# Kernel optimization log

Hardware: AMD Instinct MI355X
Metric: run time of the kernel (lower is better)

## Reference

```python
import jax, jax.numpy as jnp
import numpy as np

D_MODEL = 512; N_LAYERS = 12; D_STATE = 64; D_CONV = 4; EXPAND = 2
HEADDIM = 64; KLEN = 10
D_INNER = EXPAND * D_MODEL              # 1024
NHEADS = D_INNER // HEADDIM             # 16
CONV_DIM = D_INNER + 2 * D_STATE        # 1152
D_IN_PROJ = 2 * D_INNER + 2 * D_STATE + NHEADS  # 2192
CHUNK = 128; EPS = 1e-5
B_SZ = 2; SEQ = 2048


def rmsnorm(x, w):
    return x * jax.lax.rsqrt(jnp.mean(x * x, axis=-1, keepdims=True) + EPS) * w


def nerf_pe(x):
    # NeRF positional encoding of raw 3D coords, zero-padded to D_MODEL
    nf = D_MODEL // (2 * x.shape[-1])  # 85 freqs per coord -> 510 dims
    freqs = 2.0 ** jnp.arange(nf, dtype=x.dtype)
    ang = x[..., None] * freqs                       # [B,L,3,nf]
    pe = jnp.concatenate([jnp.sin(ang), jnp.cos(ang)], axis=-1)
    pe = pe.reshape(*x.shape[:-1], -1)               # [B,L,510]
    return jnp.pad(pe, ((0, 0), (0, 0), (0, D_MODEL - pe.shape[-1])))


def ssd(xh, dt, A, Bm, Cm):
    # Chunked Mamba2 SSD selective scan.
    # xh [B,L,H,P], dt [B,L,H] (post-softplus), A [H] (negative), Bm/Cm [B,L,N]
    Bb, L, H, P = xh.shape; N = Bm.shape[-1]; C = L // CHUNK
    xh = xh.reshape(Bb, C, CHUNK, H, P)
    dt = dt.reshape(Bb, C, CHUNK, H)
    Bm = Bm.reshape(Bb, C, CHUNK, N)
    Cm = Cm.reshape(Bb, C, CHUNK, N)
    a = dt * A                                   # [B,C,Q,H], <= 0
    a_cum = jnp.cumsum(a, axis=2)
    # intra-chunk decay L[i,j] = exp(a_cum_i - a_cum_j), i >= j
    diff = a_cum[:, :, :, None, :] - a_cum[:, :, None, :, :]  # [B,C,i,j,H]
    tri = jnp.tril(jnp.ones((CHUNK, CHUNK), bool))
    Lmat = jnp.where(tri[None, None, :, :, None], jnp.exp(diff), 0.0)
    scores = jnp.einsum('bcin,bcjn->bcij', Cm, Bm)
    M = scores[..., None] * Lmat * dt[:, :, None, :, :]       # [B,C,i,j,H]
    y_diag = jnp.einsum('bcijh,bcjhp->bcihp', M, xh)
    # per-chunk end states
    a_sum = a_cum[:, :, -1, :]                                # [B,C,H]
    dstate = jnp.exp(a_sum[:, :, None, :] - a_cum) * dt       # [B,C,Q,H]
    S = jnp.einsum('bcjh,bcjn,bcjhp->bchpn', dstate, Bm, xh)  # [B,C,H,P,N]
    dec = jnp.exp(a_sum)

    def step(h, inp):
        Sc, dc = inp
        return h * dc[:, :, None, None] + Sc, h  # emit state BEFORE this chunk

    h0 = jnp.zeros((Bb, H, P, N), xh.dtype)
    _, hs = jax.lax.scan(step, h0, (S.transpose(1, 0, 2, 3, 4), dec.transpose(1, 0, 2)))
    y_off = jnp.einsum('bcih,bcin,cbhpn->bcihp', jnp.exp(a_cum), Cm, hs)
    return (y_diag + y_off).reshape(Bb, L, H, P)


def mamba_block(x, in_w, conv_w, conv_b, dt_b, A_log, Dp, gw, out_w):
    Bb, L, _ = x.shape
    zxbcdt = x @ in_w                             # [B,L,2192]
    z = zxbcdt[..., :D_INNER]
    xBC = zxbcdt[..., D_INNER:D_INNER + CONV_DIM]
    dt = zxbcdt[..., D_INNER + CONV_DIM:]
    # causal depthwise conv1d, kernel D_CONV
    xp = jnp.pad(xBC, ((0, 0), (D_CONV - 1, 0), (0, 0)))
    xc = sum(xp[:, k:k + L, :] * conv_w[:, k] for k in range(D_CONV)) + conv_b
    xc = jax.nn.silu(xc)
    xh = xc[..., :D_INNER].reshape(Bb, L, NHEADS, HEADDIM)
    Bm = xc[..., D_INNER:D_INNER + D_STATE]
    Cm = xc[..., D_INNER + D_STATE:]
    dt = jax.nn.softplus(dt + dt_b)
    A = -jnp.exp(A_log)
    y = ssd(xh, dt, A, Bm, Cm) + Dp[None, None, :, None] * xh
    y = y.reshape(Bb, L, D_INNER)
    y = rmsnorm(y * jax.nn.silu(z), gw)           # gated RMSNorm
    return y @ out_w


def setup_inputs() -> dict:
    key = jax.random.key(0)
    ks = jax.random.split(key, 8)
    s = 0.02
    x = jax.random.normal(ks[0], (B_SZ, SEQ, 3), jnp.float32)
    W_embed = jax.random.normal(ks[1], (3, D_MODEL), jnp.float32) * s
    rms_w = jnp.ones((N_LAYERS, D_MODEL), jnp.float32)
    in_proj_w = jax.random.normal(ks[2], (N_LAYERS, D_MODEL, D_IN_PROJ), jnp.float32) * s
    conv_w = jax.random.normal(ks[3], (N_LAYERS, CONV_DIM, D_CONV), jnp.float32) * s
    conv_b = jnp.zeros((N_LAYERS, CONV_DIM), jnp.float32)
    dt_bias = jax.random.normal(ks[4], (N_LAYERS, NHEADS), jnp.float32) * 0.1
    A_log = jnp.log(jnp.broadcast_to(jnp.arange(1, NHEADS + 1, dtype=jnp.float32), (N_LAYERS, NHEADS)))
    D_param = jnp.ones((N_LAYERS, NHEADS), jnp.float32)
    gnorm_w = jnp.ones((N_LAYERS, D_INNER), jnp.float32)
    out_proj_w = jax.random.normal(ks[5], (N_LAYERS, D_INNER, D_MODEL), jnp.float32) * s
    final_norm_w = jnp.ones((D_MODEL,), jnp.float32)
    head_w = jax.random.normal(ks[6], (D_MODEL, KLEN * 3), jnp.float32) * s
    head_b = jnp.zeros((KLEN * 3,), jnp.float32)
    return dict(x=x, W_embed=W_embed, rms_w=rms_w, in_proj_w=in_proj_w,
                conv_w=conv_w, conv_b=conv_b, dt_bias=dt_bias, A_log=A_log,
                D_param=D_param, gnorm_w=gnorm_w, out_proj_w=out_proj_w,
                final_norm_w=final_norm_w, head_w=head_w, head_b=head_b)


def reference(x, W_embed, rms_w, in_proj_w, conv_w, conv_b, dt_bias, A_log,
              D_param, gnorm_w, out_proj_w, final_norm_w, head_w, head_b):
    x = jnp.where(x == -100.0, 0.0, x)            # change_maskval
    h = x @ W_embed + nerf_pe(x)                  # EmbedderAdd

    def layer(h, p):
        rw, iw, cw, cb, db, al, dp, gw, ow = p
        z = mamba_block(rmsnorm(h, rw), iw, cw, cb, db, al, dp, gw, ow)
        return h + z, None                        # dropout is identity in eval

    h, _ = jax.lax.scan(layer, h, (rms_w, in_proj_w, conv_w, conv_b, dt_bias,
                                   A_log, D_param, gnorm_w, out_proj_w))
    h = rmsnorm(h, final_norm_w)
    return h @ head_w + head_b                    # [B,L,30]
```

## Files before the change

### kernel.cpp

```cpp
#include <hip/hip_runtime.h>
#include <math.h>

#define DM 512
#define DSTATE 64
#define HD 64
#define DI 1024
#define NH 16
#define CONVD 1152
#define DIP 2192
#define CHK 128
#define NCH 16
#define BSZ 2
#define SEQL 2048
#define BL (BSZ*SEQL)
#define NLAYER 12
#define EPSF 1e-5f
#define NPAD_IN 2304

typedef __attribute__((ext_vector_type(4))) float f32x4;
typedef __attribute__((ext_vector_type(8))) short s16x8;

__device__ __forceinline__ float bf2f(ushort u) {
    union { unsigned int i; float f; } v; v.i = ((unsigned int)u) << 16; return v.f;
}
__device__ __forceinline__ ushort f2bf(float f) {
    union { float f; unsigned int u; } v; v.f = f;
    unsigned int u = v.u;
    unsigned int r = (u + 0x7fffu + ((u >> 16) & 1u)) >> 16;
    return (ushort)r;
}

#define GLOAD_LDS16(gptr, lptr) __builtin_amdgcn_global_load_lds( \
    (const __attribute__((address_space(1))) void*)(gptr), \
    (__attribute__((address_space(3))) void*)(lptr), 16, 0, 0)

#define MFMA_BF16(a, b, c) __builtin_amdgcn_mfma_f32_16x16x32_bf16(a, b, c, 0, 0, 0)

__global__ void embed_kernel(const float* __restrict__ x, const float* __restrict__ W,
                             float* __restrict__ h) {
    int tok = blockIdx.x;
    float xe[3];
#pragma unroll
    for (int e = 0; e < 3; e++) {
        float v = x[tok * 3 + e];
        xe[e] = (v == -100.0f) ? 0.0f : v;
    }
    for (int d = threadIdx.x; d < DM; d += blockDim.x) {
        float pe = 0.0f;
        if (d < 510) {
            int e = d / 170, r = d % 170;
            int is_sin = (r < 85);
            int k = is_sin ? r : r - 85;
            float ang = xe[e] * ldexpf(1.0f, k);
            double dv = is_sin ? sin((double)ang) : cos((double)ang);
            pe = (float)dv;
        }
        float acc = pe;
#pragma unroll
        for (int e = 0; e < 3; e++) acc += xe[e] * W[e * DM + d];
        h[(size_t)tok * DM + d] = acc;
    }
}

__global__ __launch_bounds__(256) void rmsnorm512_bf_kernel(const float* __restrict__ in,
                                                            const float* __restrict__ w,
                                                            ushort* __restrict__ out) {
    int tok = blockIdx.x;
    const float* row = in + (size_t)tok * DM;
    float v0 = row[threadIdx.x];
    float v1 = row[threadIdx.x + 256];
    float ss = v0 * v0 + v1 * v1;
    for (int o = 32; o; o >>= 1) ss += __shfl_down(ss, o);
    __shared__ float sbuf[4];
    if ((threadIdx.x & 63) == 0) sbuf[threadIdx.x >> 6] = ss;
    __syncthreads();
    if (threadIdx.x == 0) {
        float s = sbuf[0] + sbuf[1] + sbuf[2] + sbuf[3];
        sbuf[0] = rsqrtf(s / (float)DM + EPSF);
    }
    __syncthreads();
    float rs = sbuf[0];
    ushort* orow = out + (size_t)tok * DM;
    orow[threadIdx.x] = f2bf(v0 * rs * w[threadIdx.x]);
    orow[threadIdx.x + 256] = f2bf(v1 * rs * w[threadIdx.x + 256]);
}

__global__ __launch_bounds__(256) void gatenorm_kernel(const float* __restrict__ y,
                                                       const ushort* __restrict__ zx,
                                                       const float* __restrict__ gw,
                                                       ushort* __restrict__ yb) {
    int tok = blockIdx.x;
    const ushort* zrow = zx + (size_t)tok * DIP;
    const float* yrow = y + (size_t)tok * DI;
    float v[4];
    float ss = 0.0f;
#pragma unroll
    for (int k = 0; k < 4; k++) {
        int d = threadIdx.x + k * 256;
        float z = bf2f(zrow[d]);
        float s = z / (1.0f + __expf(-z));
        float val = yrow[d] * s;
        v[k] = val;
        ss += val * val;
    }
    for (int o = 32; o; o >>= 1) ss += __shfl_down(ss, o);
    __shared__ float sbuf[4];
    if ((threadIdx.x & 63) == 0) sbuf[threadIdx.x >> 6] = ss;
    __syncthreads();
    if (threadIdx.x == 0) {
        float s = sbuf[0] + sbuf[1] + sbuf[2] + sbuf[3];
        sbuf[0] = rsqrtf(s / (float)DI + EPSF);
    }
    __syncthreads();
    float rs = sbuf[0];
    ushort* ob = yb + (size_t)tok * DI;
#pragma unroll
    for (int k = 0; k < 4; k++) {
        int d = threadIdx.x + k * 256;
        ob[d] = f2bf(v[k] * rs * gw[d]);
    }
}

__global__ __launch_bounds__(256) void convT_kernel(const float* __restrict__ w,
                                                    ushort* __restrict__ wT,
                                                    int K, int N, int Npad) {
    __shared__ ushort tile[64][65];
    int l = blockIdx.z;
    int n0 = blockIdx.x * 64, k0 = blockIdx.y * 64;
    const float* src = w + (size_t)l * K * N;
    ushort* dst = wT + (size_t)l * Npad * K;
    int tid = threadIdx.x;
#pragma unroll
    for (int t = 0; t < 16; t++) {
        int idx = tid + t * 256;
        int r = idx >> 6, c = idx & 63;
        float v = (n0 + c < N) ? src[(size_t)(k0 + r) * N + n0 + c] : 0.0f;
        tile[c][r] = f2bf(v);
    }
    __syncthreads();
#pragma unroll
    for (int t = 0; t < 16; t++) {
        int idx = tid + t * 256;
        int r = idx >> 6, c = idx & 63;
        dst[(size_t)(n0 + r) * K + k0 + c] = tile[r][c];
    }
}

template <int MODE, int MT>
__global__ __launch_bounds__(256) void gemm_bf16_kernel(
    const ushort* __restrict__ A, const ushort* __restrict__ BT,
    ushort* __restrict__ Cb, float* __restrict__ Cf, float* __restrict__ aux,
    int N, int Nstride, int K)
{
    __shared__ ushort As[2][MT * 32 * 64];
    __shared__ ushort Bs[2][128 * 64];
    int nwg = gridDim.x * gridDim.y;
    int w0 = blockIdx.y * gridDim.x + blockIdx.x;
    int wg = (w0 & 7) * (nwg >> 3) + (w0 >> 3);
    int by = wg / gridDim.x, bx = wg - by * gridDim.x;
    int bm = by * (MT * 32), bn = bx * 128;
    int tid = threadIdx.x;
    int lane = tid & 63, wid = tid >> 6;
    int wr = wid >> 1, wc = wid & 1;
    int r15 = lane & 15, q = lane >> 4;
    f32x4 acc[MT][4] = {};
    const int nkt = K >> 6;

#define STAGE_GEMM(b, kt) do {                                              \
        int k0s = (kt) << 6;                                                \
        _Pragma("unroll")                                                   \
        for (int t = 0; t < MT; t++) {                                      \
            int cbase = wid * (MT * 64) + t * 64;                           \
            int chunk = cbase + lane;                                       \
            int row = chunk >> 3, s = chunk & 7;                            \
            int kc = s ^ (row & 7);                                         \
            GLOAD_LDS16(A + (size_t)(bm + row) * K + k0s + kc * 8,          \
                        &As[b][cbase * 8]);                                 \
        }                                                                   \
        _Pragma("unroll")                                                   \
        for (int t = 0; t < 4; t++) {                                       \
            int cbase = wid * 256 + t * 64;                                 \
            int chunk = cbase + lane;                                       \
            int row = chunk >> 3, s = chunk & 7;                            \
            int kc = s ^ (row & 7);                                         \
            GLOAD_LDS16(BT + (size_t)(bn + row) * K + k0s + kc * 8,         \
                        &Bs[b][cbase * 8]);                                 \
        }                                                                   \
    } while (0)

    STAGE_GEMM(0, 0);
    __syncthreads();
    for (int kt = 0; kt < nkt; kt++) {
        int cur = kt & 1;
        if (kt + 1 < nkt) STAGE_GEMM(cur ^ 1, kt + 1);
        const ushort* Ac = As[cur];
        const ushort* Bc = Bs[cur];
#pragma unroll
        for (int kh = 0; kh < 2; kh++) {
            s16x8 av[MT], bv[4];
#pragma unroll
            for (int m = 0; m < MT; m++) {
                int row = wr * (MT * 16) + m * 16 + r15;
                int s = (kh * 4 + q) ^ (row & 7);
                av[m] = *(const s16x8*)(Ac + row * 64 + s * 8);
            }
#pragma unroll
            for (int n = 0; n < 4; n++) {
                int row = wc * 64 + n * 16 + r15;
                int s = (kh * 4 + q) ^ (row & 7);
                bv[n] = *(const s16x8*)(Bc + row * 64 + s * 8);
            }
#pragma unroll
            for (int m = 0; m < MT; m++)
#pragma unroll
                for (int n = 0; n < 4; n++)
                    acc[m][n] = MFMA_BF16(av[m], bv[n], acc[m][n]);
        }
        __syncthreads();
    }
#undef STAGE_GEMM

#pragma unroll
    for (int m = 0; m < MT; m++) {
        int row0 = bm + wr * (MT * 16) + m * 16 + q * 4;
#pragma unroll
        for (int n = 0; n < 4; n++) {
            int col = bn + wc * 64 + n * 16 + r15;
#pragma unroll
            for (int r = 0; r < 4; r++) {
                float v = acc[m][n][r];
                int rr = row0 + r;
                if (MODE == 0) {
                    if (col < N) {
                        Cb[(size_t)rr * Nstride + col] = f2bf(v);
                        if (col >= DI + CONVD) aux[(size_t)rr * 16 + (col - DI - CONVD)] = v;
                    }
                } else if (MODE == 1) {
                    Cf[(size_t)rr * Nstride + col] += v;
                } else {
                    if (col < N) Cf[(size_t)rr * Nstride + col] = v + aux[col];
                }
            }
        }
    }
}

__global__ __launch_bounds__(256) void conv_kernel(const ushort* __restrict__ zx,
                                                   const float* __restrict__ cw,
                                                   const float* __restrict__ cb,
                                                   ushort* __restrict__ xc) {
    int gid = blockIdx.x * 256 + threadIdx.x;
    int cu = gid % (CONVD / 8);
    int rb = gid / (CONVD / 8);
    int c8 = cu * 8;
    int l0 = rb * 4;
    int lmod = l0 & (SEQL - 1);

    float wk[4][8];
    const float4* wp = (const float4*)(cw + c8 * 4);
#pragma unroll
    for (int e = 0; e < 8; e++) {
        float4 v = wp[e];
        wk[0][e] = v.x; wk[1][e] = v.y; wk[2][e] = v.z; wk[3][e] = v.w;
    }
    float4 b0 = *(const float4*)(cb + c8);
    float4 b1 = *(const float4*)(cb + c8 + 4);
    float bias[8] = {b0.x, b0.y, b0.z, b0.w, b1.x, b1.y, b1.z, b1.w};

    const ushort* base = zx + (size_t)l0 * DIP + DI + c8;
    s16x8 zero = {};
    s16x8 rows[7];
    rows[0] = (lmod >= 3) ? *(const s16x8*)(base - 3 * DIP) : zero;
    rows[1] = (lmod >= 2) ? *(const s16x8*)(base - 2 * DIP) : zero;
    rows[2] = (lmod >= 1) ? *(const s16x8*)(base - 1 * DIP) : zero;
#pragma unroll
    for (int r = 0; r < 4; r++) rows[3 + r] = *(const s16x8*)(base + (size_t)r * DIP);

    ushort* ob = xc + (size_t)l0 * CONVD + c8;
#pragma unroll
    for (int r = 0; r < 4; r++) {
        s16x8 o;
#pragma unroll
        for (int e = 0; e < 8; e++) {
            float a = bias[e];
#pragma unroll
            for (int k = 0; k < 4; k++)
                a += bf2f((ushort)rows[r + k][e]) * wk[k][e];
            float s = a / (1.0f + __expf(-a));
            o[e] = (short)f2bf(s);
        }
        *(s16x8*)(ob + (size_t)r * CONVD) = o;
    }
}

__global__ __launch_bounds__(512, 4) void ssd1_kernel(
    const ushort* __restrict__ xc, const float* __restrict__ dtraw,
    const float* __restrict__ dt_bias, const float* __restrict__ A_log,
    const float* __restrict__ Dp, float* __restrict__ acg,
    float* __restrict__ decbuf, float* __restrict__ y, float* __restrict__ S)
{
    __shared__ ushort Mb[128 * 128];
    __shared__ ushort xhT[64 * 136];
    __shared__ ushort BmT[64 * 136];
    __shared__ float sAc[128], sDt[128], sDs[128];
    __shared__ float s_wsum, s_stot;

    int hh = blockIdx.x, bc = blockIdx.y;
    int tid = threadIdx.x, lane = tid & 63, w = tid >> 6;
    int l15 = lane & 15, lq = lane >> 4;
    int bch = bc * NH + hh;
    const size_t xbase = (size_t)(bc * CHK) * CONVD;
    ushort* Cs = Mb;
    ushort* Bs = Mb + 8192;

#pragma unroll
    for (int t = 0; t < 2; t++) {
        int cbase = t * 512 + w * 64;
        int chunk = cbase + lane;
        int row = chunk >> 3, s = chunk & 7;
        int kc = s ^ (row & 7);
        GLOAD_LDS16(xc + xbase + (size_t)row * CONVD + DI + DSTATE + kc * 8, Cs + (size_t)cbase * 8);
        GLOAD_LDS16(xc + xbase + (size_t)row * CONVD + DI + kc * 8, Bs + (size_t)cbase * 8);
    }
    {
        int j = tid & 127, pc = tid >> 7;
#pragma unroll
        for (int it = 0; it < 2; it++) {
            int pc8 = pc * 2 + it;
            s16x8 vx = *(const s16x8*)(xc + xbase + (size_t)j * CONVD + hh * HD + pc8 * 8);
            s16x8 vb = *(const s16x8*)(xc + xbase + (size_t)j * CONVD + DI + pc8 * 8);
#pragma unroll
            for (int e = 0; e < 8; e++) {
                int R = pc8 * 8 + e;
                int off = R * 136 + (((j >> 3) ^ (R & 7)) << 3) + (j & 7);
                xhT[off] = (ushort)vx[e];
                BmT[off] = (ushort)vb[e];
            }
        }
    }
    float v_scan = 0.0f, dt_v = 0.0f;
    if (tid < 128) {
        float raw = dtraw[(size_t)(bc * CHK + tid) * 16 + hh] + dt_bias[hh];
        dt_v = raw > 0.0f ? raw + log1pf(__expf(-raw)) : log1pf(__expf(raw));
        v_scan = dt_v * (-__expf(A_log[hh]));
#pragma unroll
        for (int o = 1; o < 64; o <<= 1) {
            float u = __shfl_up(v_scan, o);
            if (lane >= o) v_scan += u;
        }
        if (tid == 63) s_wsum = v_scan;
    }
    __syncthreads();

    float ac_v = 0.0f;
    if (tid < 128) {
        ac_v = (tid >= 64) ? v_scan + s_wsum : v_scan;
        if (tid == 127) s_stot = ac_v;
    }
    f32x4 acc_s[8] = {};
    {
        int row = w * 16 + l15;
#pragma unroll
        for (int kh = 0; kh < 2; kh++) {
            int sl = (kh * 4 + lq) ^ (row & 7);
            s16x8 av = *(const s16x8*)(Cs + row * 64 + sl * 8);
#pragma unroll
            for (int nj = 0; nj < 8; nj++) {
                int jr = nj * 16 + l15;
                int sl2 = (kh * 4 + lq) ^ (jr & 7);
                s16x8 bv = *(const s16x8*)(Bs + jr * 64 + sl2 * 8);
                acc_s[nj] = MFMA_BF16(av, bv, acc_s[nj]);
            }
        }
    }
    __syncthreads();

    if (tid < 128) {
        float asum = s_stot;
        sAc[tid] = ac_v;
        sDt[tid] = dt_v;
        sDs[tid] = __expf(asum - ac_v) * dt_v;
        acg[(size_t)bch * CHK + tid] = ac_v;
        if (tid == 0) decbuf[bch] = __expf(asum);
    }
    __syncthreads();

#pragma unroll
    for (int nj = 0; nj < 8; nj++) {
        int j = nj * 16 + l15;
        if (nj < w) {
            float acj = sAc[j], dtj = sDt[j];
#pragma unroll
            for (int r = 0; r < 4; r++) {
                int i = w * 16 + lq * 4 + r;
                float v = acc_s[nj][r] * __expf(sAc[i] - acj) * dtj;
                Mb[i * 128 + ((((i & 7) ^ (j >> 3)) << 3) | (j & 7))] = f2bf(v);
            }
        } else if (nj == w) {
            float acj = sAc[j], dtj = sDt[j];
#pragma unroll
            for (int r = 0; r < 4; r++) {
                int i = w * 16 + lq * 4 + r;
                float v = (j <= i) ? acc_s[nj][r] * __expf(sAc[i] - acj) * dtj : 0.0f;
                Mb[i * 128 + ((((i & 7) ^ (j >> 3)) << 3) | (j & 7))] = f2bf(v);
            }
        } else if (nj == w + 1) {
#pragma unroll
            for (int r = 0; r < 4; r++) {
                int i = w * 16 + lq * 4 + r;
                Mb[i * 128 + ((((i & 7) ^ (j >> 3)) << 3) | (j & 7))] = 0;
            }
        }
    }
    __syncthreads();

    int ph = w >> 2, iq = w & 3;
    f32x4 acc_y[2][2] = {};
    f32x4 acc_st[2] = {};
    int nn = iq * 16 + l15;
#pragma unroll
    for (int ks = 0; ks < 4; ks++) {
        int cj = ks * 4 + lq;
        int j0 = ks * 32 + lq * 8;
        s16x8 axh[2], axs[2];
#pragma unroll
        for (int m = 0; m < 2; m++) {
            int p = ph * 32 + m * 16 + l15;
            axh[m] = *(const s16x8*)(xhT + p * 136 + ((cj ^ (p & 7)) << 3));
            s16x8 r;
#pragma unroll
            for (int e = 0; e < 8; e++)
                r[e] = (short)f2bf(bf2f((ushort)axh[m][e]) * sDs[j0 + e]);
            axs[m] = r;
        }
        s16x8 bb = *(const s16x8*)(BmT + nn * 136 + ((cj ^ (nn & 7)) << 3));
#pragma unroll
        for (int m = 0; m < 2; m++)
            acc_st[m] = MFMA_BF16(axs[m], bb, acc_st[m]);
        if (ks <= iq) {
            s16x8 bm_[2];
#pragma unroll
            for (int n = 0; n < 2; n++) {
                int i = iq * 32 + n * 16 + l15;
                bm_[n] = *(const s16x8*)(Mb + i * 128 + ((cj ^ (i & 7)) << 3));
            }
#pragma unroll
            for (int m = 0; m < 2; m++)
#pragma unroll
                for (int n = 0; n < 2; n++)
                    acc_y[m][n] = MFMA_BF16(axh[m], bm_[n], acc_y[m][n]);
        }
    }

    float Dh = Dp[hh];
#pragma unroll
    for (int m = 0; m < 2; m++) {
        int p0 = ph * 32 + m * 16 + lq * 4;
#pragma unroll
        for (int n = 0; n < 2; n++) {
            int i = iq * 32 + n * 16 + l15;
            f32x4 v = acc_y[m][n];
#pragma unroll
            for (int r = 0; r < 4; r++) {
                int p = p0 + r;
                v[r] += Dh * bf2f(xhT[p * 136 + ((((p & 7) ^ (i >> 3)) << 3) | (i & 7))]);
            }
            *(f32x4*)&y[(size_t)(bc * CHK + i) * DI + hh * HD + p0] = v;
        }
#pragma unroll
        for (int r = 0; r < 4; r++)
            S[(size_t)bch * 4096 + (size_t)(p0 + r) * 64 + nn] = acc_st[m][r];
    }
}

__global__ void scan_kernel(const float* __restrict__ S, const float* __restrict__ decbuf,
                            float* __restrict__ hs) {
    int g = blockIdx.x * 256 + threadIdx.x;
    int n = g & 63, p = (g >> 6) & 63, hh = (g >> 12) & 15, b = g >> 16;
    float state = 0.0f;
#pragma unroll
    for (int c = 0; c < NCH; c++) {
        int bch = (b * NCH + c) * NH + hh;
        size_t idx = (size_t)bch * 4096 + p * 64 + n;
        hs[idx] = state;
        state = state * decbuf[bch] + S[idx];
    }
}

__global__ __launch_bounds__(256) void ssd2_kernel(
    const ushort* __restrict__ xc, const float* __restrict__ hsg,
    const float* __restrict__ acg, float* __restrict__ y)
{
    __shared__ ushort Cs[128 * 64];
    __shared__ ushort Hs[64 * 64];
    __shared__ float sAc[128];
    int hh = blockIdx.x, bc = blockIdx.y;
    int tid = threadIdx.x, lane = tid & 63, wid = tid >> 6;
    int wr = wid >> 1, wc = wid & 1, l15 = lane & 15, lq = lane >> 4;
    int bch = bc * NH + hh;
    const size_t xbase = (size_t)(bc * CHK) * CONVD;
#pragma unroll
    for (int t = 0; t < 4; t++) {
        int cbase = t * 256 + wid * 64;
        int chunk = cbase + lane;
        int row = chunk >> 3, s = chunk & 7;
        int kc = s ^ (row & 7);
        GLOAD_LDS16(xc + xbase + (size_t)row * CONVD + DI + DSTATE + kc * 8, Cs + (size_t)cbase * 8);
    }
#pragma unroll
    for (int t = 0; t < 2; t++) {
        int chunk = t * 256 + tid;
        int p = chunk >> 3, s = chunk & 7;
        int kc = s ^ (p & 7);
        const float* src = hsg + (size_t)bch * 4096 + p * 64 + kc * 8;
        ushort* dst = Hs + p * 64 + s * 8;
#pragma unroll
        for (int e = 0; e < 8; e++) dst[e] = f2bf(src[e]);
    }
    if (tid < 128) sAc[tid] = acg[(size_t)bch * CHK + tid];
    __syncthreads();
    f32x4 acc[2][4] = {};
#pragma unroll
    for (int kh = 0; kh < 2; kh++) {
        s16x8 av[2], bv[4];
#pragma unroll
        for (int m = 0; m < 2; m++) {
            int p = wr * 32 + m * 16 + l15;
            int sl = (kh * 4 + lq) ^ (p & 7);
            av[m] = *(const s16x8*)(Hs + p * 64 + sl * 8);
        }
#pragma unroll
        for (int n = 0; n < 4; n++) {
            int i = wc * 64 + n * 16 + l15;
            int sl = (kh * 4 + lq) ^ (i & 7);
            bv[n] = *(const s16x8*)(Cs + i * 64 + sl * 8);
        }
#pragma unroll
        for (int m = 0; m < 2; m++)
#pragma unroll
            for (int n = 0; n < 4; n++)
                acc[m][n] = MFMA_BF16(av[m], bv[n], acc[m][n]);
    }
#pragma unroll
    for (int m = 0; m < 2; m++) {
        int p0 = wr * 32 + m * 16 + lq * 4;
#pragma unroll
        for (int n = 0; n < 4; n++) {
            int i = wc * 64 + n * 16 + l15;
            float e = __expf(sAc[i]);
            float* dst = &y[(size_t)(bc * CHK + i) * DI + hh * HD + p0];
            f32x4 v = *(f32x4*)dst;
#pragma unroll
            for (int r = 0; r < 4; r++) v[r] += e * acc[m][n][r];
            *(f32x4*)dst = v;
        }
    }
}

extern "C" void kernel_launch(void* const* d_in, const int* in_sizes, int n_in,
                              void* d_out, int out_size, void* d_ws, size_t ws_size,
                              hipStream_t stream) {
    const float* x        = (const float*)d_in[0];
    const float* W_embed  = (const float*)d_in[1];
    const float* rms_w    = (const float*)d_in[2];
    const float* in_w     = (const float*)d_in[3];
    const float* conv_w   = (const float*)d_in[4];
    const float* conv_b   = (const float*)d_in[5];
    const float* dt_bias  = (const float*)d_in[6];
    const float* A_log    = (const float*)d_in[7];
    const float* D_param  = (const float*)d_in[8];
    const float* gnorm_w  = (const float*)d_in[9];
    const float* out_w    = (const float*)d_in[10];
    const float* fnorm_w  = (const float*)d_in[11];
    const float* head_w   = (const float*)d_in[12];
    const float* head_b   = (const float*)d_in[13];
    float* out = (float*)d_out;

    char* p = (char*)d_ws;
    auto alloc = [&](size_t bytes) { char* r = p; p += (bytes + 255) & ~(size_t)255; return r; };

    float*  h_buf   = (float*)alloc((size_t)BL * DM * 4);
    float*  y_buf   = (float*)alloc((size_t)BL * DI * 4);
    float*  S_buf   = (float*)alloc((size_t)BSZ * NCH * NH * HD * DSTATE * 4);
    float*  hs_buf  = (float*)alloc((size_t)BSZ * NCH * NH * HD * DSTATE * 4);
    float*  ac_buf  = (float*)alloc((size_t)BSZ * NCH * NH * CHK * 4);
    float*  dec_buf = (float*)alloc((size_t)BSZ * NCH * NH * 4);
    float*  dtraw   = (float*)alloc((size_t)BL * 16 * 4);
    ushort* xn_bf   = (ushort*)alloc((size_t)BL * DM * 2);
    ushort* zx_bf   = (ushort*)alloc((size_t)BL * DIP * 2);
    ushort* xc_bf   = (ushort*)alloc((size_t)BL * CONVD * 2);
    ushort* y_bf    = (ushort*)alloc((size_t)BL * DI * 2);
    ushort* headT   = (ushort*)alloc((size_t)128 * DM * 2);

    size_t in_full  = (size_t)NLAYER * NPAD_IN * DM * 2;
    size_t out_full = (size_t)NLAYER * DM * DI * 2;
    size_t used = (size_t)(p - (char*)d_ws);
    bool full = (used + in_full + out_full + 4096) <= ws_size;
    ushort* inT  = (ushort*)alloc(full ? in_full  : (size_t)NPAD_IN * DM * 2);
    ushort* outT = (ushort*)alloc(full ? out_full : (size_t)DM * DI * 2);

    embed_kernel<<<BL, 256, 0, stream>>>(x, W_embed, h_buf);
    convT_kernel<<<dim3(2, DM / 64, 1), 256, 0, stream>>>(head_w, headT, DM, 30, 128);
    if (full) {
        convT_kernel<<<dim3(NPAD_IN / 64, DM / 64, NLAYER), 256, 0, stream>>>(
            in_w, inT, DM, DIP, NPAD_IN);
        convT_kernel<<<dim3(DM / 64, DI / 64, NLAYER), 256, 0, stream>>>(
            out_w, outT, DI, DM, DM);
    }

    for (int l = 0; l < NLAYER; l++) {
        const float* rw = rms_w + (size_t)l * DM;
        const float* cw = conv_w + (size_t)l * CONVD * 4;
        const float* cb = conv_b + (size_t)l * CONVD;
        const float* db = dt_bias + (size_t)l * NH;
        const float* al = A_log + (size_t)l * NH;
        const float* dp = D_param + (size_t)l * NH;
        const float* gw = gnorm_w + (size_t)l * DI;

        ushort* inT_l  = full ? inT  + (size_t)l * NPAD_IN * DM : inT;
        ushort* outT_l = full ? outT + (size_t)l * DM * DI      : outT;
        if (!full) {
            convT_kernel<<<dim3(NPAD_IN / 64, DM / 64, 1), 256, 0, stream>>>(
                in_w + (size_t)l * DM * DIP, inT_l, DM, DIP, NPAD_IN);
            convT_kernel<<<dim3(DM / 64, DI / 64, 1), 256, 0, stream>>>(
                out_w + (size_t)l * DI * DM, outT_l, DI, DM, DM);
        }

        rmsnorm512_bf_kernel<<<BL, 256, 0, stream>>>(h_buf, rw, xn_bf);
        gemm_bf16_kernel<0, 2><<<dim3(NPAD_IN / 128, BL / 64), 256, 0, stream>>>(
            xn_bf, inT_l, zx_bf, nullptr, dtraw, DIP, DIP, DM);
        conv_kernel<<<((BL / 4) * (CONVD / 8)) / 256, 256, 0, stream>>>(zx_bf, cw, cb, xc_bf);
        ssd1_kernel<<<dim3(NH, BSZ * NCH), 512, 0, stream>>>(xc_bf, dtraw, db, al, dp,
                                                             ac_buf, dec_buf, y_buf, S_buf);
        scan_kernel<<<(BSZ * NH * HD * DSTATE) / 256, 256, 0, stream>>>(S_buf, dec_buf,
                                                                        hs_buf);
        ssd2_kernel<<<dim3(NH, BSZ * NCH), 256, 0, stream>>>(xc_bf, hs_buf, ac_buf, y_buf);
        gatenorm_kernel<<<BL, 256, 0, stream>>>(y_buf, zx_bf, gw, y_bf);
        gemm_bf16_kernel<1, 1><<<dim3(DM / 128, BL / 32), 256, 0, stream>>>(
            y_bf, outT_l, nullptr, h_buf, nullptr, DM, DM, DI);
    }

    rmsnorm512_bf_kernel<<<BL, 256, 0, stream>>>(h_buf, fnorm_w, xn_bf);
    gemm_bf16_kernel<2, 4><<<dim3(1, BL / 128), 256, 0, stream>>>(
        xn_bf, headT, nullptr, out, (float*)head_b, 30, 30, DM);
}
```

Before: 1.244 ms.

## Fuse inter-chunk scan into ssd2 and fold D skip into M diagonal

Removes the separate scan kernel launch. Each ssd2 block now recomputes its incoming chunk state directly by summing prior chunk states weighted by cumulative decays, which drops the hs buffer write and read. In ssd1, the D skip term is folded into the diagonal of the intra-chunk M matrix, and the dstate scaling is applied once to BmT in LDS instead of per-MFMA on x. This costs redundant reads of S in later chunks (up to 15 per block), and adding D on the diagonal in bf16 may change precision slightly.

After: 1.249 ms. About the same (+0.4%).

```diff
diff --git a/kernel.cpp b/kernel.cpp
--- a/kernel.cpp
+++ b/kernel.cpp
@@ -312,6 +312,7 @@
     const size_t xbase = (size_t)(bc * CHK) * CONVD;
     ushort* Cs = Mb;
     ushort* Bs = Mb + 8192;
+    float Dh = Dp[hh];
 
 #pragma unroll
     for (int t = 0; t < 2; t++) {
@@ -401,7 +402,10 @@
 #pragma unroll
             for (int r = 0; r < 4; r++) {
                 int i = w * 16 + lq * 4 + r;
-                float v = (j <= i) ? acc_s[nj][r] * __expf(sAc[i] - acj) * dtj : 0.0f;
+                float v;
+                if (j < i)       v = acc_s[nj][r] * __expf(sAc[i] - acj) * dtj;
+                else if (j == i) v = acc_s[nj][r] * dtj + Dh;
+                else             v = 0.0f;
                 Mb[i * 128 + ((((i & 7) ^ (j >> 3)) << 3) | (j & 7))] = f2bf(v);
             }
         } else if (nj == w + 1) {
@@ -410,6 +414,16 @@
                 int i = w * 16 + lq * 4 + r;
                 Mb[i * 128 + ((((i & 7) ^ (j >> 3)) << 3) | (j & 7))] = 0;
             }
+        }
+    }
+    {
+        int j = tid & 127, g = tid >> 7;
+        float dsj = sDs[j];
+#pragma unroll
+        for (int rr = 0; rr < 16; rr++) {
+            int R = g * 16 + rr;
+            int off = R * 136 + (((j >> 3) ^ (R & 7)) << 3) + (j & 7);
+            BmT[off] = f2bf(bf2f(BmT[off]) * dsj);
         }
     }
     __syncthreads();
@@ -421,22 +435,16 @@
 #pragma unroll
     for (int ks = 0; ks < 4; ks++) {
         int cj = ks * 4 + lq;
-        int j0 = ks * 32 + lq * 8;
-        s16x8 axh[2], axs[2];
+        s16x8 axh[2];
 #pragma unroll
         for (int m = 0; m < 2; m++) {
             int p = ph * 32 + m * 16 + l15;
             axh[m] = *(const s16x8*)(xhT + p * 136 + ((cj ^ (p & 7)) << 3));
-            s16x8 r;
-#pragma unroll
-            for (int e = 0; e < 8; e++)
-                r[e] = (short)f2bf(bf2f((ushort)axh[m][e]) * sDs[j0 + e]);
-            axs[m] = r;
         }
         s16x8 bb = *(const s16x8*)(BmT + nn * 136 + ((cj ^ (nn & 7)) << 3));
 #pragma unroll
         for (int m = 0; m < 2; m++)
-            acc_st[m] = MFMA_BF16(axs[m], bb, acc_st[m]);
+            acc_st[m] = MFMA_BF16(axh[m], bb, acc_st[m]);
         if (ks <= iq) {
             s16x8 bm_[2];
 #pragma unroll
@@ -452,20 +460,13 @@
         }
     }
 
-    float Dh = Dp[hh];
 #pragma unroll
     for (int m = 0; m < 2; m++) {
         int p0 = ph * 32 + m * 16 + lq * 4;
 #pragma unroll
         for (int n = 0; n < 2; n++) {
             int i = iq * 32 + n * 16 + l15;
-            f32x4 v = acc_y[m][n];
-#pragma unroll
-            for (int r = 0; r < 4; r++) {
-                int p = p0 + r;
-                v[r] += Dh * bf2f(xhT[p * 136 + ((((p & 7) ^ (i >> 3)) << 3) | (i & 7))]);
-            }
-            *(f32x4*)&y[(size_t)(bc * CHK + i) * DI + hh * HD + p0] = v;
+            *(f32x4*)&y[(size_t)(bc * CHK + i) * DI + hh * HD + p0] = acc_y[m][n];
         }
 #pragma unroll
         for (int r = 0; r < 4; r++)
@@ -473,23 +474,10 @@
     }
 }
 
-__global__ void scan_kernel(const float* __restrict__ S, const float* __restrict__ decbuf,
-                            float* __restrict__ hs) {
-    int g = blockIdx.x * 256 + threadIdx.x;
-    int n = g & 63, p = (g >> 6) & 63, hh = (g >> 12) & 15, b = g >> 16;
-    float state = 0.0f;
-#pragma unroll
-    for (int c = 0; c < NCH; c++) {
-        int bch = (b * NCH + c) * NH + hh;
-        size_t idx = (size_t)bch * 4096 + p * 64 + n;
-        hs[idx] = state;
-        state = state * decbuf[bch] + S[idx];
-    }
-}
-
 __global__ __launch_bounds__(256) void ssd2_kernel(
-    const ushort* __restrict__ xc, const float* __restrict__ hsg,
-    const float* __restrict__ acg, float* __restrict__ y)
+    const ushort* __restrict__ xc, const float* __restrict__ Sg,
+    const float* __restrict__ decg, const float* __restrict__ acg,
+    float* __restrict__ y)
 {
     __shared__ ushort Cs[128 * 64];
     __shared__ ushort Hs[64 * 64];
@@ -498,6 +486,7 @@
     int tid = threadIdx.x, lane = tid & 63, wid = tid >> 6;
     int wr = wid >> 1, wc = wid & 1, l15 = lane & 15, lq = lane >> 4;
     int bch = bc * NH + hh;
+    int b = bc >> 4, cc = bc & 15;
     const size_t xbase = (size_t)(bc * CHK) * CONVD;
 #pragma unroll
     for (int t = 0; t < 4; t++) {
@@ -507,15 +496,33 @@
         int kc = s ^ (row & 7);
         GLOAD_LDS16(xc + xbase + (size_t)row * CONVD + DI + DSTATE + kc * 8, Cs + (size_t)cbase * 8);
     }
-#pragma unroll
-    for (int t = 0; t < 2; t++) {
-        int chunk = t * 256 + tid;
-        int p = chunk >> 3, s = chunk & 7;
-        int kc = s ^ (p & 7);
-        const float* src = hsg + (size_t)bch * 4096 + p * 64 + kc * 8;
-        ushort* dst = Hs + p * 64 + s * 8;
-#pragma unroll
-        for (int e = 0; e < 8; e++) dst[e] = f2bf(src[e]);
+    {
+        int p = tid >> 2, n0 = (tid & 3) * 16;
+        f32x4 acc4[4] = {};
+        float wgt = 1.0f;
+        for (int c = cc - 1; c >= 0; --c) {
+            int bch_c = (b * NCH + c) * NH + hh;
+            const float* src = Sg + (size_t)bch_c * 4096 + p * 64 + n0;
+            float dv = decg[bch_c];
+#pragma unroll
+            for (int q2 = 0; q2 < 4; q2++) {
+                f32x4 sv = *(const f32x4*)(src + q2 * 4);
+                acc4[q2].x += sv.x * wgt; acc4[q2].y += sv.y * wgt;
+                acc4[q2].z += sv.z * wgt; acc4[q2].w += sv.w * wgt;
+            }
+            wgt *= dv;
+        }
+#pragma unroll
+        for (int g = 0; g < 2; g++) {
+            int nch = (n0 >> 3) + g;
+            int s = nch ^ (p & 7);
+            ushort* dst = Hs + p * 64 + s * 8;
+#pragma unroll
+            for (int ee = 0; ee < 8; ee++) {
+                int idx = g * 8 + ee;
+                dst[ee] = f2bf(acc4[idx >> 2][idx & 3]);
+            }
+        }
     }
     if (tid < 128) sAc[tid] = acg[(size_t)bch * CHK + tid];
     __syncthreads();
@@ -582,7 +589,6 @@
     float*  h_buf   = (float*)alloc((size_t)BL * DM * 4);
     float*  y_buf   = (float*)alloc((size_t)BL * DI * 4);
     float*  S_buf   = (float*)alloc((size_t)BSZ * NCH * NH * HD * DSTATE * 4);
-    float*  hs_buf  = (float*)alloc((size_t)BSZ * NCH * NH * HD * DSTATE * 4);
     float*  ac_buf  = (float*)alloc((size_t)BSZ * NCH * NH * CHK * 4);
     float*  dec_buf = (float*)alloc((size_t)BSZ * NCH * NH * 4);
     float*  dtraw   = (float*)alloc((size_t)BL * 16 * 4);
@@ -632,9 +638,8 @@
         conv_kernel<<<((BL / 4) * (CONVD / 8)) / 256, 256, 0, stream>>>(zx_bf, cw, cb, xc_bf);
         ssd1_kernel<<<dim3(NH, BSZ * NCH), 512, 0, stream>>>(xc_bf, dtraw, db, al, dp,
                                                              ac_buf, dec_buf, y_buf, S_buf);
-        scan_kernel<<<(BSZ * NH * HD * DSTATE) / 256, 256, 0, stream>>>(S_buf, dec_buf,
-                                                                        hs_buf);
-        ssd2_kernel<<<dim3(NH, BSZ * NCH), 256, 0, stream>>>(xc_bf, hs_buf, ac_buf, y_buf);
+        ssd2_kernel<<<dim3(NH, BSZ * NCH), 256, 0, stream>>>(xc_bf, S_buf, dec_buf,
+                                                             ac_buf, y_buf);
         gatenorm_kernel<<<BL, 256, 0, stream>>>(y_buf, zx_bf, gw, y_bf);
         gemm_bf16_kernel<1, 1><<<dim3(DM / 128, BL / 32), 256, 0, stream>>>(
             y_bf, outT_l, nullptr, h_buf, nullptr, DM, DM, DI);
```
